# Kernel tuning notes

Hardware: AMD Instinct MI355X
Metric: run time of the kernel (lower is better)

## Reference

```python
import jax, jax.numpy as jnp
import numpy as np

B, T, D, H = 512, 128, 128, 256


def _uniform(key, shape, fan):
    s = 1.0 / np.sqrt(fan)
    return jax.random.uniform(key, shape, minval=-s, maxval=s, dtype=jnp.float32)


def setup_inputs() -> dict:
    key = jax.random.key(0)
    ks = jax.random.split(key, 16)
    return {
        "x": jax.random.normal(ks[0], (B, T, D), jnp.float32),
        "mask": jax.random.randint(ks[1], (B, T, D), 0, 2).astype(jnp.int32),
        # nn.LSTMCell(2D, H): weights init U(-1/sqrt(H), 1/sqrt(H))
        "W_ih": _uniform(ks[2], (4 * H, 2 * D), H),
        "W_hh": _uniform(ks[3], (4 * H, H), H),
        "b_ih": _uniform(ks[4], (4 * H,), H),
        "b_hh": _uniform(ks[5], (4 * H,), H),
        # TemporalDecay h: W [H, D], stdv = 1/sqrt(W.size(0)) = 1/sqrt(H)
        "W_dh": _uniform(ks[6], (H, D), H),
        "b_dh": _uniform(ks[7], (H,), H),
        # TemporalDecay x (diag): W [D, D]
        "W_dx": _uniform(ks[8], (D, D), D),
        "b_dx": _uniform(ks[9], (D,), D),
        # hist_reg Linear(H, D): torch default U(-1/sqrt(H), 1/sqrt(H))
        "W_hr": _uniform(ks[10], (D, H), H),
        "b_hr": _uniform(ks[11], (D,), H),
        "W_fr": _uniform(ks[12], (D, D), D),
        "b_fr": _uniform(ks[13], (D,), D),
        # weight_combine Linear(2D, D)
        "W_wc": _uniform(ks[14], (D, 2 * D), 2 * D),
        "b_wc": _uniform(ks[15], (D,), 2 * D),
    }


def _compute_delta(m_tm):
    # m_tm: [T, B, D] float; delta[0]=0, delta[t]=m[t-1] + (1-m[t-1])*(delta[t-1]+1)
    Tn, Bn, Dn = m_tm.shape
    def step(prev, m_prev):
        new = m_prev + (1.0 - m_prev) * (prev + 1.0)
        return new, new
    _, rest = jax.lax.scan(step, jnp.zeros((Bn, Dn), m_tm.dtype), m_tm[:-1])
    return jnp.concatenate([jnp.zeros((1, Bn, Dn), m_tm.dtype), rest], axis=0)


def _rits_forward(x, mask, W_ih, W_hh, b_ih, b_hh, W_dh, b_dh, W_dx, b_dx,
                  W_hr, b_hr, W_fr, b_fr, W_wc, b_wc):
    Bn, Tn, Dn = x.shape
    Hn = W_hh.shape[1]
    m = mask.astype(x.dtype)
    x_tm = jnp.swapaxes(x, 0, 1)   # [T,B,D]
    m_tm = jnp.swapaxes(m, 0, 1)   # [T,B,D]
    deltas = _compute_delta(m_tm)  # [T,B,D]

    W_fr_masked = W_fr * (1.0 - jnp.eye(Dn, dtype=x.dtype))  # zero diagonal
    dx_diag = jnp.diag(W_dx)  # diag-masked linear == elementwise scale

    def step(carry, inputs):
        h, c = carry
        xt, mt, dt = inputs
        gamma_h = jnp.exp(-jax.nn.relu(dt @ W_dh.T + b_dh))      # [B,H]
        gamma_x = jnp.exp(-jax.nn.relu(dt * dx_diag + b_dx))     # [B,D]
        h = h * gamma_h
        x_h = h @ W_hr.T + b_hr                                  # [B,D]
        x_c = jnp.where(mt > 0, xt, x_h)
        z_h = x_c @ W_fr_masked.T + b_fr                         # [B,D]
        alpha = jnp.concatenate([gamma_x, mt], axis=1) @ W_wc.T + b_wc
        c_h = alpha * z_h + (1.0 - alpha) * x_h
        c_c = jnp.where(mt > 0, xt, c_h)
        lstm_in = jnp.concatenate([c_c, mt], axis=1)             # [B,2D]
        gates = lstm_in @ W_ih.T + b_ih + h @ W_hh.T + b_hh      # [B,4H]
        i, f, g, o = jnp.split(gates, 4, axis=1)
        c_new = jax.nn.sigmoid(f) * c + jax.nn.sigmoid(i) * jnp.tanh(g)
        h_new = jax.nn.sigmoid(o) * jnp.tanh(c_new)
        return (h_new, c_new), (x_h, z_h, c_h)

    init = (jnp.zeros((Bn, Hn), x.dtype), jnp.zeros((Bn, Hn), x.dtype))
    _, (first, second, third) = jax.lax.scan(step, init, (x_tm, m_tm, deltas))
    first = jnp.swapaxes(first, 0, 1)
    second = jnp.swapaxes(second, 0, 1)
    third = jnp.swapaxes(third, 0, 1)
    return first, second, third, third  # x_out == third (both are c_h)


def reference(x, mask, W_ih, W_hh, b_ih, b_hh, W_dh, b_dh, W_dx, b_dx,
              W_hr, b_hr, W_fr, b_fr, W_wc, b_wc):
    return _rits_forward(x, mask, W_ih, W_hh, b_ih, b_hh, W_dh, b_dh,
                         W_dx, b_dx, W_hr, b_hr, W_fr, b_fr, W_wc, b_wc)
```

## Files before the change

kernel.cpp:

```cpp
#include <hip/hip_runtime.h>

typedef unsigned short u16;
typedef unsigned int u32;
typedef unsigned long long u64;
typedef __attribute__((ext_vector_type(8))) short s16x8;
typedef __attribute__((ext_vector_type(4))) float f32x4;

#define MFMA16(a, b, c) __builtin_amdgcn_mfma_f32_16x16x32_bf16((a), (b), (c), 0, 0, 0)

static constexpr int Bn = 512, Tn = 128, Dn = 128, Hn = 256;
static constexpr int NG = 4 * Hn;
static constexpr int KG = 2 * Dn + Hn;
static constexpr long long BTD = (long long)Bn * Tn * Dn;

__device__ __forceinline__ u16 f2bf(float f) {
  union { float f; unsigned u; } v; v.f = f;
  unsigned u = v.u;
  return (u16)((u + 0x7fffu + ((u >> 16) & 1u)) >> 16);
}
__device__ __forceinline__ float bf2f(u16 h) {
  union { unsigned u; float f; } v; v.u = ((unsigned)h) << 16;
  return v.f;
}
__device__ __forceinline__ float sigm(float x) {
  return __builtin_amdgcn_rcpf(1.f + __expf(-x));
}
__device__ __forceinline__ float ftanh(float x) {
  return 1.f - 2.f * __builtin_amdgcn_rcpf(1.f + __expf(2.f * x));
}

__global__ void k_pack(const float* __restrict__ W_ih, const float* __restrict__ W_hh,
                       const float* __restrict__ W_hr, const float* __restrict__ W_fr,
                       const float* __restrict__ W_dh, const float* __restrict__ W_wc,
                       u16* Wg, u16* Whr_b, u16* Wfr_b, u16* Wdh_b, u16* Wwc_b) {
  int i = blockIdx.x * 256 + threadIdx.x;
  if (i < NG * KG) {
    int n = i >> 9, k = i & 511;
    float v = (k < 256) ? W_ih[n * 256 + k] : W_hh[n * 256 + (k - 256)];
    Wg[i] = f2bf(v);
  }
  if (i < Dn * Hn) Whr_b[i] = f2bf(W_hr[i]);
  if (i < Dn * Dn) {
    int r = i >> 7, c = i & 127;
    Wfr_b[i] = f2bf(r == c ? 0.f : W_fr[i]);
  }
  if (i < Hn * Dn) Wdh_b[i] = f2bf(W_dh[i]);
  if (i < Dn * Hn) Wwc_b[i] = f2bf(W_wc[i]);
}

__global__ void k_delta(const float* __restrict__ x, const int* __restrict__ mask,
                        const float* __restrict__ W_dx, const float* __restrict__ b_dx,
                        u16* delta_bf, u16* gx_bf, u16* m_bf, u16* x_bf) {
  int idx = blockIdx.x * 256 + threadIdx.x;
  int b = idx >> 7, d = idx & 127;
  float dxd = W_dx[d * Dn + d], bxd = b_dx[d];
  float del = 0.f;
  const float* xrow = x + (long long)b * Tn * Dn + d;
  const int* mrow = mask + (long long)b * Tn * Dn + d;
  for (int t0 = 0; t0 < Tn; t0 += 4) {
    float xv[4]; int mv[4];
#pragma unroll
    for (int k = 0; k < 4; ++k) {
      xv[k] = xrow[(t0 + k) * Dn];
      mv[k] = mrow[(t0 + k) * Dn];
    }
#pragma unroll
    for (int k = 0; k < 4; ++k) {
      int t = t0 + k;
      long long o = ((long long)t * Bn + b) * Dn + d;
      delta_bf[o] = f2bf(del);
      gx_bf[o] = f2bf(__expf(-fmaxf(del * dxd + bxd, 0.f)));
      float m = (float)mv[k];
      m_bf[o] = f2bf(m);
      x_bf[o] = f2bf(xv[k]);
      del = m + (1.f - m) * (del + 1.f);
    }
  }
}

__global__ void k_ga(const u16* __restrict__ delta_bf, const u16* __restrict__ gx_bf,
                     const u16* __restrict__ m_bf,
                     const u16* __restrict__ Wdh_b, const u16* __restrict__ Wwc_b,
                     const float* __restrict__ b_dh, const float* __restrict__ b_wc,
                     u16* __restrict__ gammah, u16* __restrict__ alpha) {
  int tid = threadIdx.x, wid = tid >> 6, l = tid & 63;
  int lr = l & 15, lg = l >> 4;
  if (blockIdx.x < 4096) {
    int bid = blockIdx.x;
    int t = bid >> 5, b0 = (bid & 31) << 4;
    const u16* Arow = delta_bf + ((long long)t * Bn + b0) * Dn;
    s16x8 afr[4];
#pragma unroll
    for (int ks = 0; ks < 4; ++ks)
      afr[ks] = *(const s16x8*)(Arow + (long long)lr * Dn + ks * 32 + lg * 8);
#pragma unroll
    for (int q = 0; q < 4; ++q) {
      int n0 = (wid * 4 + q) * 16;
      f32x4 acc = {0.f, 0.f, 0.f, 0.f};
#pragma unroll
      for (int ks = 0; ks < 4; ++ks) {
        s16x8 bfr = *(const s16x8*)(Wdh_b + (long long)(n0 + lr) * Dn + ks * 32 + lg * 8);
        acc = MFMA16(afr[ks], bfr, acc);
      }
      int n = n0 + lr;
      float bb = b_dh[n];
#pragma unroll
      for (int r = 0; r < 4; ++r) {
        int row = lg * 4 + r;
        float g = __expf(-fmaxf(acc[r] + bb, 0.f));
        gammah[((long long)t * Bn + b0 + row) * Hn + n] = f2bf(g);
      }
    }
  } else {
    int bid = blockIdx.x - 4096;
    int t = bid >> 5, b0 = (bid & 31) << 4;
    s16x8 afr[8];
#pragma unroll
    for (int ks = 0; ks < 8; ++ks) {
      const u16* src = (ks < 4) ? gx_bf : m_bf;
      int kk = (ks & 3) * 32 + lg * 8;
      afr[ks] = *(const s16x8*)(src + ((long long)t * Bn + b0 + lr) * Dn + kk);
    }
#pragma unroll
    for (int q = 0; q < 2; ++q) {
      int n0 = (wid * 2 + q) * 16;
      f32x4 acc = {0.f, 0.f, 0.f, 0.f};
#pragma unroll
      for (int ks = 0; ks < 8; ++ks) {
        s16x8 bfr = *(const s16x8*)(Wwc_b + (long long)(n0 + lr) * (2 * Dn) + ks * 32 + lg * 8);
        acc = MFMA16(afr[ks], bfr, acc);
      }
      int n = n0 + lr;
      float bb = b_wc[n];
#pragma unroll
      for (int r = 0; r < 4; ++r)
        alpha[((long long)t * Bn + b0 + lg * 4 + r) * Dn + n] = f2bf(acc[r] + bb);
    }
  }
}

__global__ __launch_bounds__(512) void k_main(
    const u16* __restrict__ x_bf, const u16* __restrict__ m_bf,
    const u16* __restrict__ Wg, const u16* __restrict__ Whr_b, const u16* __restrict__ Wfr_b,
    const u16* __restrict__ gammah, const u16* __restrict__ alpha,
    const float* __restrict__ b_ih, const float* __restrict__ b_hh,
    const float* __restrict__ b_hr, const float* __restrict__ b_fr,
    float* __restrict__ out, u64* __restrict__ Hex, int* __restrict__ flags) {
  __shared__ __align__(16) u16 A_lds[64 * 128];
  __shared__ __align__(16) u16 Axc[16 * 128];
  __shared__ __align__(16) float G_lds[16 * 128];

  const int tid = threadIdx.x, wid = tid >> 6, l = tid & 63;
  const int lr = l & 15, lg = l >> 4;
  const int g = blockIdx.x & 31, s = blockIdx.x >> 5;
  const int b0 = g * 16;

  for (int i = tid; i < 32 * 128; i += 512) A_lds[32 * 128 + i] = 0;

  const int dd = wid * 16 + lr;
  const float bhr = b_hr[dd], bfr = b_fr[dd];

  const int prow = tid >> 5, pjj = tid & 31;
  const int pj = 32 * s + pjj;
  const float bg0 = b_ih[0 * 256 + pj] + b_hh[0 * 256 + pj];
  const float bg1 = b_ih[1 * 256 + pj] + b_hh[1 * 256 + pj];
  const float bg2 = b_ih[2 * 256 + pj] + b_hh[2 * 256 + pj];
  const float bg3 = b_ih[3 * 256 + pj] + b_hh[3 * 256 + pj];

  s16x8 whr[8], wfr[4], wg[16];
#pragma unroll
  for (int ks = 0; ks < 8; ++ks)
    whr[ks] = *(const s16x8*)(Whr_b + (long long)dd * Hn + ks * 32 + lg * 8);
#pragma unroll
  for (int ks = 0; ks < 4; ++ks)
    wfr[ks] = *(const s16x8*)(Wfr_b + (long long)dd * Dn + ks * 32 + lg * 8);
  {
    const int q = wid >> 1;
    const long long grow = q * 256 + 32 * s + 16 * (wid & 1) + lr;
#pragma unroll
    for (int ks = 0; ks < 16; ++ks)
      wg[ks] = *(const s16x8*)(Wg + grow * KG + ks * 32 + lg * 8);
  }

  const u16* a_base = A_lds + lg * 128 + lr * 8;
  const u16* axc_base = Axc + lg * 128 + lr * 8;

  float cst = 0.f;
  float xn[4], mnv[4], an[4];
#pragma unroll
  for (int r = 0; r < 4; ++r) {
    int row = lg * 4 + r;
    long long o = ((long long)0 * Bn + b0 + row) * Dn + dd;
    xn[r] = bf2f(x_bf[o]); mnv[r] = bf2f(m_bf[o]); an[r] = bf2f(alpha[o]);
  }

  float* out0 = out;
  float* out1 = out + BTD;
  float* out2 = out + 2 * BTD;
  float* out3 = out + 3 * BTD;

#pragma unroll 1
  for (int t = 0; t < Tn; ++t) {
    __syncthreads();
    float gmh = 1.f;
    if (t + 1 < Tn)
      gmh = bf2f(gammah[((long long)(t + 1) * Bn + b0 + prow) * Hn + pj]);

    f32x4 acc = {0.f, 0.f, 0.f, 0.f};
#pragma unroll
    for (int ks = 0; ks < 8; ++ks) {
      s16x8 a = *(const s16x8*)(a_base + 32 * 128 + ks * 512);
      acc = MFMA16(a, whr[ks], acc);
    }
    float xh[4], xv[4], av[4], mv[4];
#pragma unroll
    for (int r = 0; r < 4; ++r) {
      int row = lg * 4 + r;
      xh[r] = acc[r] + bhr;
      xv[r] = xn[r]; mv[r] = mnv[r]; av[r] = an[r];
      float xc = (mv[r] > 0.5f) ? xv[r] : xh[r];
      Axc[(dd >> 3) * 128 + row * 8 + (dd & 7)] = f2bf(xc);
      A_lds[(16 + (dd >> 3)) * 128 + row * 8 + (dd & 7)] = f2bf(mv[r]);
    }
    __syncthreads();

    acc = f32x4{0.f, 0.f, 0.f, 0.f};
#pragma unroll
    for (int ks = 0; ks < 4; ++ks) {
      s16x8 a = *(const s16x8*)(axc_base + ks * 512);
      acc = MFMA16(a, wfr[ks], acc);
    }
    float zv[4], chv[4];
#pragma unroll
    for (int r = 0; r < 4; ++r) {
      int row = lg * 4 + r;
      zv[r] = acc[r] + bfr;
      chv[r] = av[r] * zv[r] + (1.f - av[r]) * xh[r];
      float ccv = (mv[r] > 0.5f) ? xv[r] : chv[r];
      A_lds[(dd >> 3) * 128 + row * 8 + (dd & 7)] = f2bf(ccv);
    }
    __syncthreads();

    if (t + 1 < Tn) {
#pragma unroll
      for (int r = 0; r < 4; ++r) {
        int row = lg * 4 + r;
        long long o = ((long long)(t + 1) * Bn + b0 + row) * Dn + dd;
        xn[r] = bf2f(x_bf[o]); mnv[r] = bf2f(m_bf[o]); an[r] = bf2f(alpha[o]);
      }
    }
    acc = f32x4{0.f, 0.f, 0.f, 0.f};
#pragma unroll
    for (int ks = 0; ks < 16; ++ks) {
      s16x8 a = *(const s16x8*)(a_base + ks * 512);
      acc = MFMA16(a, wg[ks], acc);
    }
#pragma unroll
    for (int r = 0; r < 4; ++r)
      G_lds[(lg * 4 + r) * 128 + wid * 16 + lr] = acc[r];
    __syncthreads();

    float gi = G_lds[prow * 128 + 0 * 32 + pjj] + bg0;
    float gf = G_lds[prow * 128 + 1 * 32 + pjj] + bg1;
    float gg = G_lds[prow * 128 + 2 * 32 + pjj] + bg2;
    float go = G_lds[prow * 128 + 3 * 32 + pjj] + bg3;
    float iv = sigm(gi), fv = sigm(gf), gv = ftanh(gg), ov = sigm(go);
    cst = fv * cst + iv * gv;
    float h = ov * ftanh(cst);

    if (t + 1 < Tn) {
      unsigned hv = (unsigned)f2bf(h * gmh);
      unsigned up = (unsigned)__shfl_xor((int)hv, 1);
      u32* HexW = (u32*)(Hex + (size_t)((t + 1) & 1) * 32768 + (size_t)g * 1024);
      if (!(tid & 1))
        __hip_atomic_store(HexW + (prow * 128 + 16 * s + (pjj >> 1)), hv | (up << 16),
                           __ATOMIC_RELAXED, __HIP_MEMORY_SCOPE_AGENT);
      __syncthreads();
      if (tid == 0)
        __hip_atomic_store(flags + (((g << 3) | s) << 5), t + 1,
                           __ATOMIC_RELAXED, __HIP_MEMORY_SCOPE_AGENT);
    }

    if (wid == s) {
#pragma unroll
      for (int r = 0; r < 4; ++r) {
        int row = lg * 4 + r;
        long long gx = ((long long)(b0 + row) * Tn + t) * Dn + dd;
        out0[gx] = xh[r];
        out1[gx] = zv[r];
        out2[gx] = chv[r];
        out3[gx] = chv[r];
      }
    }

    if (t + 1 < Tn) {
      const int target = t + 1;
      int v;
      do {
        v = (l < 8)
            ? __hip_atomic_load(flags + (((g << 3) | l) << 5),
                                __ATOMIC_RELAXED, __HIP_MEMORY_SCOPE_AGENT)
            : target;
      } while (!__all(v >= target));
      const u64* HexR = Hex + (size_t)((t + 1) & 1) * 32768 + (size_t)g * 1024;
      int row = tid & 15, c = tid >> 4;
      u64 w0 = __hip_atomic_load(HexR + row * 64 + c * 2,
                                 __ATOMIC_RELAXED, __HIP_MEMORY_SCOPE_AGENT);
      u64 w1 = __hip_atomic_load(HexR + row * 64 + c * 2 + 1,
                                 __ATOMIC_RELAXED, __HIP_MEMORY_SCOPE_AGENT);
      u64* dst = (u64*)(A_lds + (32 + c) * 128 + row * 8);
      dst[0] = w0; dst[1] = w1;
    }
  }
}

extern "C" void kernel_launch(void* const* d_in, const int* in_sizes, int n_in,
                              void* d_out, int out_size, void* d_ws, size_t ws_size,
                              hipStream_t stream) {
  (void)in_sizes; (void)n_in; (void)out_size; (void)ws_size;
  const float* x = (const float*)d_in[0];
  const int* mask = (const int*)d_in[1];
  const float* W_ih = (const float*)d_in[2];
  const float* W_hh = (const float*)d_in[3];
  const float* b_ih = (const float*)d_in[4];
  const float* b_hh = (const float*)d_in[5];
  const float* W_dh = (const float*)d_in[6];
  const float* b_dh = (const float*)d_in[7];
  const float* W_dx = (const float*)d_in[8];
  const float* b_dx = (const float*)d_in[9];
  const float* W_hr = (const float*)d_in[10];
  const float* b_hr = (const float*)d_in[11];
  const float* W_fr = (const float*)d_in[12];
  const float* b_fr = (const float*)d_in[13];
  const float* W_wc = (const float*)d_in[14];
  const float* b_wc = (const float*)d_in[15];

  char* ws = (char*)d_ws;
  size_t off = 0;
  auto alloc = [&](size_t bytes) {
    void* p = ws + off;
    off = (off + bytes + 255) & ~(size_t)255;
    return p;
  };
  const long long TBD = (long long)Tn * Bn * Dn;
  const long long TBH = (long long)Tn * Bn * Hn;
  u16* delta_bf = (u16*)alloc(TBD * 2);
  u16* gx_bf    = (u16*)alloc(TBD * 2);
  u16* m_bf     = (u16*)alloc(TBD * 2);
  u16* x_bf     = (u16*)alloc(TBD * 2);
  u16* gammah   = (u16*)alloc(TBH * 2);
  u16* alphaw   = (u16*)alloc(TBD * 2);
  u16* Wg    = (u16*)alloc((size_t)NG * KG * 2);
  u16* Whr_b = (u16*)alloc((size_t)Dn * Hn * 2);
  u16* Wfr_b = (u16*)alloc((size_t)Dn * Dn * 2);
  u16* Wdh_b = (u16*)alloc((size_t)Hn * Dn * 2);
  u16* Wwc_b = (u16*)alloc((size_t)Dn * Hn * 2);

  u64* Hex = (u64*)delta_bf;
  int* flags = (int*)((char*)delta_bf + 512 * 1024);

  k_pack<<<2048, 256, 0, stream>>>(W_ih, W_hh, W_hr, W_fr, W_dh, W_wc,
                                   Wg, Whr_b, Wfr_b, Wdh_b, Wwc_b);
  k_delta<<<(Bn * Dn) / 256, 256, 0, stream>>>(x, mask, W_dx, b_dx,
                                               delta_bf, gx_bf, m_bf, x_bf);
  k_ga<<<8192, 256, 0, stream>>>(delta_bf, gx_bf, m_bf, Wdh_b, Wwc_b,
                                 b_dh, b_wc, gammah, alphaw);
  hipMemsetAsync(flags, 0, 256 * 128, stream);

  void* args[] = {
    (void*)&x_bf, (void*)&m_bf, (void*)&Wg, (void*)&Whr_b, (void*)&Wfr_b,
    (void*)&gammah, (void*)&alphaw, (void*)&b_ih, (void*)&b_hh,
    (void*)&b_hr, (void*)&b_fr, (void*)&d_out, (void*)&Hex, (void*)&flags
  };
  hipLaunchCooperativeKernel((const void*)k_main, dim3(256), dim3(512), args, 0, stream);
}
```

Before: 573.8 us.

## Merge prep kernels, vectorize delta pass, and split cross-block h exchange per wave

Folds the weight-packing and delta/decay kernels into one launch, and has each delta thread handle two features with paired 32-bit stores so accesses are wider. In the recurrent cooperative kernel, each block writes its own h slice straight into LDS. Each of the other waves then spins only on its matching producer's flag and copies just that slice, replacing the single whole-block wait on all eight flags. This is meant to cut launch overhead and per-step synchronization latency, at the cost of more intricate per-wave ordering with a higher risk of subtle races.

```diff
diff --git a/kernel.cpp b/kernel.cpp
--- a/kernel.cpp
+++ b/kernel.cpp
@@ -29,51 +29,58 @@
   return 1.f - 2.f * __builtin_amdgcn_rcpf(1.f + __expf(2.f * x));
 }
 
-__global__ void k_pack(const float* __restrict__ W_ih, const float* __restrict__ W_hh,
+__global__ void k_prep(const float* __restrict__ W_ih, const float* __restrict__ W_hh,
                        const float* __restrict__ W_hr, const float* __restrict__ W_fr,
                        const float* __restrict__ W_dh, const float* __restrict__ W_wc,
-                       u16* Wg, u16* Whr_b, u16* Wfr_b, u16* Wdh_b, u16* Wwc_b) {
-  int i = blockIdx.x * 256 + threadIdx.x;
-  if (i < NG * KG) {
-    int n = i >> 9, k = i & 511;
-    float v = (k < 256) ? W_ih[n * 256 + k] : W_hh[n * 256 + (k - 256)];
-    Wg[i] = f2bf(v);
-  }
-  if (i < Dn * Hn) Whr_b[i] = f2bf(W_hr[i]);
-  if (i < Dn * Dn) {
-    int r = i >> 7, c = i & 127;
-    Wfr_b[i] = f2bf(r == c ? 0.f : W_fr[i]);
-  }
-  if (i < Hn * Dn) Wdh_b[i] = f2bf(W_dh[i]);
-  if (i < Dn * Hn) Wwc_b[i] = f2bf(W_wc[i]);
-}
-
-__global__ void k_delta(const float* __restrict__ x, const int* __restrict__ mask,
-                        const float* __restrict__ W_dx, const float* __restrict__ b_dx,
-                        u16* delta_bf, u16* gx_bf, u16* m_bf, u16* x_bf) {
-  int idx = blockIdx.x * 256 + threadIdx.x;
-  int b = idx >> 7, d = idx & 127;
-  float dxd = W_dx[d * Dn + d], bxd = b_dx[d];
-  float del = 0.f;
+                       const float* __restrict__ x, const int* __restrict__ mask,
+                       const float* __restrict__ W_dx, const float* __restrict__ b_dx,
+                       u16* Wg, u16* Whr_b, u16* Wfr_b, u16* Wdh_b, u16* Wwc_b,
+                       u16* delta_bf, u16* gx_bf, u16* m_bf, u16* x_bf) {
+  if (blockIdx.x < 2048) {
+    int i = blockIdx.x * 256 + threadIdx.x;
+    if (i < NG * KG) {
+      int n = i >> 9, k = i & 511;
+      float v = (k < 256) ? W_ih[n * 256 + k] : W_hh[n * 256 + (k - 256)];
+      Wg[i] = f2bf(v);
+    }
+    if (i < Dn * Hn) Whr_b[i] = f2bf(W_hr[i]);
+    if (i < Dn * Dn) {
+      int r = i >> 7, c = i & 127;
+      Wfr_b[i] = f2bf(r == c ? 0.f : W_fr[i]);
+    }
+    if (i < Hn * Dn) Wdh_b[i] = f2bf(W_dh[i]);
+    if (i < Dn * Hn) Wwc_b[i] = f2bf(W_wc[i]);
+    return;
+  }
+  int idx = (blockIdx.x - 2048) * 256 + threadIdx.x;
+  int b = idx >> 6, dp = idx & 63, d = dp * 2;
+  float dxd0 = W_dx[d * Dn + d], dxd1 = W_dx[(d + 1) * Dn + (d + 1)];
+  float bxd0 = b_dx[d], bxd1 = b_dx[d + 1];
+  float del0 = 0.f, del1 = 0.f;
   const float* xrow = x + (long long)b * Tn * Dn + d;
   const int* mrow = mask + (long long)b * Tn * Dn + d;
+  u32* d32 = (u32*)delta_bf; u32* g32 = (u32*)gx_bf;
+  u32* m32 = (u32*)m_bf; u32* x32 = (u32*)x_bf;
   for (int t0 = 0; t0 < Tn; t0 += 4) {
-    float xv[4]; int mv[4];
+    float2 xv[4]; int2 mv[4];
 #pragma unroll
     for (int k = 0; k < 4; ++k) {
-      xv[k] = xrow[(t0 + k) * Dn];
-      mv[k] = mrow[(t0 + k) * Dn];
+      xv[k] = *(const float2*)(xrow + (t0 + k) * Dn);
+      mv[k] = *(const int2*)(mrow + (t0 + k) * Dn);
     }
 #pragma unroll
     for (int k = 0; k < 4; ++k) {
       int t = t0 + k;
-      long long o = ((long long)t * Bn + b) * Dn + d;
-      delta_bf[o] = f2bf(del);
-      gx_bf[o] = f2bf(__expf(-fmaxf(del * dxd + bxd, 0.f)));
-      float m = (float)mv[k];
-      m_bf[o] = f2bf(m);
-      x_bf[o] = f2bf(xv[k]);
-      del = m + (1.f - m) * (del + 1.f);
+      long long o2 = (((long long)t * Bn + b) * Dn + d) >> 1;
+      d32[o2] = (u32)f2bf(del0) | ((u32)f2bf(del1) << 16);
+      float gx0 = __expf(-fmaxf(del0 * dxd0 + bxd0, 0.f));
+      float gx1 = __expf(-fmaxf(del1 * dxd1 + bxd1, 0.f));
+      g32[o2] = (u32)f2bf(gx0) | ((u32)f2bf(gx1) << 16);
+      float m0 = (float)mv[k].x, m1 = (float)mv[k].y;
+      m32[o2] = (u32)f2bf(m0) | ((u32)f2bf(m1) << 16);
+      x32[o2] = (u32)f2bf(xv[k].x) | ((u32)f2bf(xv[k].y) << 16);
+      del0 = m0 + (1.f - m0) * (del0 + 1.f);
+      del1 = m1 + (1.f - m1) * (del1 + 1.f);
     }
   }
 }
@@ -275,6 +282,7 @@
       if (!(tid & 1))
         __hip_atomic_store(HexW + (prow * 128 + 16 * s + (pjj >> 1)), hv | (up << 16),
                            __ATOMIC_RELAXED, __HIP_MEMORY_SCOPE_AGENT);
+      A_lds[(32 + (pj >> 3)) * 128 + prow * 8 + (pj & 7)] = (u16)hv;
       __syncthreads();
       if (tid == 0)
         __hip_atomic_store(flags + (((g << 3) | s) << 5), t + 1,
@@ -293,21 +301,18 @@
       }
     }
 
-    if (t + 1 < Tn) {
+    if (t + 1 < Tn && wid != s) {
       const int target = t + 1;
+      const int* fp = flags + (((g << 3) | wid) << 5);
       int v;
       do {
-        v = (l < 8)
-            ? __hip_atomic_load(flags + (((g << 3) | l) << 5),
-                                __ATOMIC_RELAXED, __HIP_MEMORY_SCOPE_AGENT)
-            : target;
-      } while (!__all(v >= target));
-      const u64* HexR = Hex + (size_t)((t + 1) & 1) * 32768 + (size_t)g * 1024;
-      int row = tid & 15, c = tid >> 4;
-      u64 w0 = __hip_atomic_load(HexR + row * 64 + c * 2,
-                                 __ATOMIC_RELAXED, __HIP_MEMORY_SCOPE_AGENT);
-      u64 w1 = __hip_atomic_load(HexR + row * 64 + c * 2 + 1,
-                                 __ATOMIC_RELAXED, __HIP_MEMORY_SCOPE_AGENT);
+        v = __hip_atomic_load(fp, __ATOMIC_RELAXED, __HIP_MEMORY_SCOPE_AGENT);
+      } while (v < target);
+      const int row = l & 15, c = 4 * wid + (l >> 4);
+      const u64* rp = Hex + (size_t)((t + 1) & 1) * 32768 + (size_t)g * 1024
+                      + (row * 64 + c * 2);
+      u64 w0 = __hip_atomic_load(rp, __ATOMIC_RELAXED, __HIP_MEMORY_SCOPE_AGENT);
+      u64 w1 = __hip_atomic_load(rp + 1, __ATOMIC_RELAXED, __HIP_MEMORY_SCOPE_AGENT);
       u64* dst = (u64*)(A_lds + (32 + c) * 128 + row * 8);
       dst[0] = w0; dst[1] = w1;
     }
@@ -359,10 +364,10 @@
   u64* Hex = (u64*)delta_bf;
   int* flags = (int*)((char*)delta_bf + 512 * 1024);
 
-  k_pack<<<2048, 256, 0, stream>>>(W_ih, W_hh, W_hr, W_fr, W_dh, W_wc,
-                                   Wg, Whr_b, Wfr_b, Wdh_b, Wwc_b);
-  k_delta<<<(Bn * Dn) / 256, 256, 0, stream>>>(x, mask, W_dx, b_dx,
-                                               delta_bf, gx_bf, m_bf, x_bf);
+  k_prep<<<2176, 256, 0, stream>>>(W_ih, W_hh, W_hr, W_fr, W_dh, W_wc,
+                                   x, mask, W_dx, b_dx,
+                                   Wg, Whr_b, Wfr_b, Wdh_b, Wwc_b,
+                                   delta_bf, gx_bf, m_bf, x_bf);
   k_ga<<<8192, 256, 0, stream>>>(delta_bf, gx_bf, m_bf, Wdh_b, Wwc_b,
                                  b_dh, b_wc, gammah, alphaw);
   hipMemsetAsync(flags, 0, 256 * 128, stream);
```

Result: slower. 595.1 us (+3.7%).
